# Kernel tuning notes

Measured on AMD Instinct MI355X. Metric: run time of the kernel, lower is better.

The kernel has to match this reference:

```python
import jax, jax.numpy as jnp
import numpy as np

B, S, D, O, C = 4, 2048, 1024, 1024, 8


def setup_inputs() -> dict:
    key = jax.random.key(0)
    k1, k2, k3, k4 = jax.random.split(key, 4)
    x = jax.random.normal(k1, (B, S, D), dtype=jnp.float32)
    category_id = jax.random.randint(k2, (B, S), 0, C, dtype=jnp.int64)
    weight = jax.random.normal(k3, (C, D, O), dtype=jnp.float32)
    bias = jax.random.normal(k4, (C, O), dtype=jnp.float32)
    return {"x": x, "category_id": category_id, "weight": weight, "bias": bias}


def reference(x, category_id, weight, bias):
    # Faithful to: out[t] = x[t] @ weight[cid[t]] + bias[cid[t]]
    # Instead of gathering a full [T, D, O] weight tensor per token (32GB),
    # compute every category's projection once and select per token.
    orig_shape = x.shape
    x_flat = x.reshape(-1, orig_shape[-1])          # [T, D]
    cid = category_id.reshape(-1)                    # [T]
    out_all = jnp.einsum('td,cdo->tco', x_flat, weight)  # [T, C, O]
    out = jnp.take_along_axis(out_all, cid[:, None, None], axis=1)[:, 0, :]  # [T, O]
    out = out + bias[cid]
    return out.reshape(orig_shape[:-1] + (weight.shape[-1],))
```

## Files before the change

### kernel.cpp

```cpp
#include <hip/hip_runtime.h>

#define TOK   8192
#define DIM   1024
#define OUTD  1024
#define NCAT  8
#define BM    128
#define BN    128
#define BK    32
#define NKT   (DIM / BK)
#define MAX_MT 71
#define MPMAX (MAX_MT * BM)

typedef __attribute__((ext_vector_type(8))) __bf16 bf16x8;
typedef __attribute__((ext_vector_type(4))) float  f32x4;

__device__ __forceinline__ unsigned short f2bf(float f) {
  unsigned u = __float_as_uint(f);
  u += 0x7fffu + ((u >> 16) & 1u);
  return (unsigned short)(u >> 16);
}

__global__ __launch_bounds__(1024) void k_build(const int* __restrict__ cid,
    int* __restrict__ row_token, int* __restrict__ tile_c, int* __restrict__ tile_m) {
  __shared__ int wcnt[16][NCAT];
  __shared__ int wbase[16][NCAT];
  __shared__ int gbase[NCAT];
  int tid = threadIdx.x, lane = tid & 63, wave = tid >> 6;
  int base = wave * 512;

  int cs[8];
  #pragma unroll
  for (int it = 0; it < 8; ++it) cs[it] = cid[base + it * 64 + lane];
  int cnt_loc[NCAT];
  #pragma unroll
  for (int c = 0; c < NCAT; ++c) cnt_loc[c] = 0;
  #pragma unroll
  for (int it = 0; it < 8; ++it) {
    #pragma unroll
    for (int c = 0; c < NCAT; ++c) {
      unsigned long long m = __ballot(cs[it] == c);
      cnt_loc[c] += __popcll(m);
    }
  }
  if (lane == 0) {
    #pragma unroll
    for (int c = 0; c < NCAT; ++c) wcnt[wave][c] = cnt_loc[c];
  }
  __syncthreads();

  if (tid == 0) {
    int pr = 0, mt = 0;
    for (int c = 0; c < NCAT; ++c) {
      int tot = 0;
      for (int w = 0; w < 16; ++w) { wbase[w][c] = tot; tot += wcnt[w][c]; }
      gbase[c] = pr;
      int nt = (tot + BM - 1) / BM;
      for (int i = 0; i < nt; ++i) { tile_c[mt] = c; tile_m[mt] = pr + i * BM; ++mt; }
      pr += nt * BM;
    }
    for (; mt < MAX_MT; ++mt) { tile_c[mt] = -1; tile_m[mt] = 0; }
  }
  __syncthreads();
  for (int r = tid; r < MPMAX; r += 1024) row_token[r] = -1;
  __syncthreads();

  int run[NCAT];
  #pragma unroll
  for (int c = 0; c < NCAT; ++c) run[c] = gbase[c] + wbase[wave][c];
  unsigned long long lt = (lane == 63) ? ~0ull >> 1 : ((1ull << lane) - 1);
  #pragma unroll
  for (int it = 0; it < 8; ++it) {
    int t = base + it * 64 + lane;
    int c = cs[it];
    int pos = 0;
    #pragma unroll
    for (int cat = 0; cat < NCAT; ++cat) {
      unsigned long long m = __ballot(cs[it] == cat);
      if (cat == c) pos = run[cat] + __popcll(m & lt);
      run[cat] += __popcll(m);
    }
    row_token[pos] = t;
  }
}

__global__ __launch_bounds__(256) void k_convert(const float* __restrict__ w,
    const float* __restrict__ x, const int* __restrict__ row_token,
    unsigned short* __restrict__ wt, unsigned short* __restrict__ xg) {
  int tid = threadIdx.x;
  if (blockIdx.x < 2048) {
    int b = blockIdx.x;
    int ot = b & 15, dt = (b >> 4) & 15, c = b >> 8;
    __shared__ unsigned short t[64][72];
    int i  = tid >> 2;
    int jg = tid & 3;
    const float* src = w + ((size_t)c << 20) + (size_t)(dt * 64 + i) * 1024 + ot * 64 + jg * 16;
    #pragma unroll
    for (int q = 0; q < 4; ++q) {
      float4 v = *(const float4*)(src + q * 4);
      t[jg * 16 + q * 4 + 0][i] = f2bf(v.x);
      t[jg * 16 + q * 4 + 1][i] = f2bf(v.y);
      t[jg * 16 + q * 4 + 2][i] = f2bf(v.z);
      t[jg * 16 + q * 4 + 3][i] = f2bf(v.w);
    }
    __syncthreads();
    unsigned short* dst = wt + ((size_t)c << 20) + (size_t)(ot * 64 + i) * 1024 + dt * 64 + jg * 16;
    uint4 a = *(const uint4*)&t[i][jg * 16];
    uint4 bq = *(const uint4*)&t[i][jg * 16 + 8];
    *(uint4*)dst = a;
    *(uint4*)(dst + 8) = bq;
  } else {
    int idx = (blockIdx.x - 2048) * 256 + tid;
    int r  = idx >> 7;
    int e0 = (idx & 127) << 3;
    if (r >= MPMAX) return;
    int tok = row_token[r];
    union { unsigned short u[8]; uint4 v; } o;
    if (tok >= 0) {
      const float4* s = (const float4*)(x + (size_t)tok * DIM + e0);
      float4 a = s[0], b = s[1];
      o.u[0] = f2bf(a.x); o.u[1] = f2bf(a.y); o.u[2] = f2bf(a.z); o.u[3] = f2bf(a.w);
      o.u[4] = f2bf(b.x); o.u[5] = f2bf(b.y); o.u[6] = f2bf(b.z); o.u[7] = f2bf(b.w);
    } else {
      o.v = make_uint4(0u, 0u, 0u, 0u);
    }
    *(uint4*)(xg + (size_t)r * DIM + e0) = o.v;
  }
}

__global__ __launch_bounds__(256) void k_gemm(const unsigned short* __restrict__ xg,
    const unsigned short* __restrict__ wt, const float* __restrict__ bias,
    const int* __restrict__ row_token, const int* __restrict__ tile_c,
    const int* __restrict__ tile_m, float* __restrict__ out) {
  int wg  = blockIdx.x;
  int lin = (wg & 7) * MAX_MT + (wg >> 3);
  int mt  = lin >> 3;
  int nt  = lin & 7;
  int c = tile_c[mt];
  if (c < 0) return;
  int m0 = tile_m[mt];
  int n0 = nt * BN;

  __shared__ unsigned short As[3][BM][BK];
  __shared__ unsigned short Bs[3][BM][BK];

  int tid  = threadIdx.x;
  int lane = tid & 63;
  int wr = (tid >> 6) >> 1, wc = (tid >> 6) & 1;

  f32x4 acc[4][4];
  #pragma unroll
  for (int m = 0; m < 4; ++m)
    #pragma unroll
    for (int n = 0; n < 4; ++n) acc[m][n] = (f32x4){0.f, 0.f, 0.f, 0.f};

  const unsigned short* Ag = xg + (size_t)m0 * DIM;
  const unsigned short* Bg = wt + ((size_t)c << 20) + (size_t)n0 * DIM;

  int srow = tid >> 2;
  int sdst = (tid & 3) << 3;
  int gsrc = (((tid & 3) ^ ((tid >> 3) & 3)) << 3);

  auto STAGE = [&](int b, int kt) {
    __builtin_amdgcn_global_load_lds(
      (const __attribute__((address_space(1))) unsigned int*)(Ag + (size_t)srow * DIM + kt + gsrc),
      (__attribute__((address_space(3))) unsigned int*)(&As[b][srow][sdst]), 16, 0, 0);
    __builtin_amdgcn_global_load_lds(
      (const __attribute__((address_space(1))) unsigned int*)(Ag + (size_t)(srow + 64) * DIM + kt + gsrc),
      (__attribute__((address_space(3))) unsigned int*)(&As[b][srow + 64][sdst]), 16, 0, 0);
    __builtin_amdgcn_global_load_lds(
      (const __attribute__((address_space(1))) unsigned int*)(Bg + (size_t)srow * DIM + kt + gsrc),
      (__attribute__((address_space(3))) unsigned int*)(&Bs[b][srow][sdst]), 16, 0, 0);
    __builtin_amdgcn_global_load_lds(
      (const __attribute__((address_space(1))) unsigned int*)(Bg + (size_t)(srow + 64) * DIM + kt + gsrc),
      (__attribute__((address_space(3))) unsigned int*)(&Bs[b][srow + 64][sdst]), 16, 0, 0);
  };

  int rcol = (((lane >> 4) ^ ((lane & 15) >> 1 & 3)) << 3);
  int arow = wr * 64 + (lane & 15);
  int brow = wc * 64 + (lane & 15);

  STAGE(0, 0); STAGE(1, BK); STAGE(2, 2 * BK);

  int b = 0;
  for (int t = 0; t < NKT; ++t) {
    if (t < NKT - 2)       asm volatile("s_waitcnt vmcnt(8)" ::: "memory");
    else if (t == NKT - 2) asm volatile("s_waitcnt vmcnt(4)" ::: "memory");
    else                   asm volatile("s_waitcnt vmcnt(0)" ::: "memory");
    __builtin_amdgcn_s_barrier();

    bf16x8 af[4], bf[4];
    #pragma unroll
    for (int m = 0; m < 4; ++m)
      af[m] = *(const bf16x8*)&As[b][arow + m * 16][rcol];
    #pragma unroll
    for (int n = 0; n < 4; ++n)
      bf[n] = *(const bf16x8*)&Bs[b][brow + n * 16][rcol];
    #pragma unroll
    for (int m = 0; m < 4; ++m)
      #pragma unroll
      for (int n = 0; n < 4; ++n)
        acc[m][n] = __builtin_amdgcn_mfma_f32_16x16x32_bf16(af[m], bf[n], acc[m][n], 0, 0, 0);

    __builtin_amdgcn_s_barrier();
    if (t < NKT - 3) STAGE(b, (t + 3) * BK);
    b = (b == 2) ? 0 : b + 1;
  }

  int col = lane & 15;
  int rq  = (lane >> 4) << 2;
  float bv[4];
  #pragma unroll
  for (int n = 0; n < 4; ++n) bv[n] = bias[c * OUTD + n0 + wc * 64 + n * 16 + col];
  #pragma unroll
  for (int m = 0; m < 4; ++m) {
    #pragma unroll
    for (int r = 0; r < 4; ++r) {
      int prow = m0 + wr * 64 + m * 16 + rq + r;
      int tok = row_token[prow];
      if (tok < 0) continue;
      float* orow = out + (size_t)tok * OUTD + n0 + wc * 64 + col;
      #pragma unroll
      for (int n = 0; n < 4; ++n) orow[n * 16] = acc[m][n][r] + bv[n];
    }
  }
}

extern "C" void kernel_launch(void* const* d_in, const int* in_sizes, int n_in,
                              void* d_out, int out_size, void* d_ws, size_t ws_size,
                              hipStream_t stream) {
  const float* x    = (const float*)d_in[0];
  const int*   cid  = (const int*)d_in[1];
  const float* w    = (const float*)d_in[2];
  const float* bias = (const float*)d_in[3];
  float* out = (float*)d_out;

  char* ws = (char*)d_ws;
  constexpr size_t XG_BYTES = (size_t)MPMAX * DIM * 2;
  constexpr size_t WT_BYTES = (size_t)NCAT * DIM * OUTD * 2;
  constexpr size_t RT_BYTES = (size_t)MPMAX * 4;
  unsigned short* xg  = (unsigned short*)ws;
  unsigned short* wtb = (unsigned short*)(ws + XG_BYTES);
  int* row_token = (int*)(ws + XG_BYTES + WT_BYTES);
  int* tile_c    = (int*)(ws + XG_BYTES + WT_BYTES + RT_BYTES);
  int* tile_m    = tile_c + MAX_MT;

  k_build<<<1, 1024, 0, stream>>>(cid, row_token, tile_c, tile_m);
  k_convert<<<2048 + (MPMAX * (DIM / 8) + 255) / 256, 256, 0, stream>>>(w, x, row_token, wtb, xg);
  k_gemm<<<8 * MAX_MT, 256, 0, stream>>>(xg, wtb, bias, row_token, tile_c, tile_m, out);
}
```

Baseline: 151.0 us.

## Fuse x gather and bf16 conversion into GEMM A-tile loads, merge prep kernels

New measurement: 177.9 us. 17.8% more time.

```diff
diff --git a/kernel.cpp b/kernel.cpp
--- a/kernel.cpp
+++ b/kernel.cpp
@@ -20,72 +20,9 @@
   return (unsigned short)(u >> 16);
 }
 
-__global__ __launch_bounds__(1024) void k_build(const int* __restrict__ cid,
+__global__ __launch_bounds__(256) void k_prep(const float* __restrict__ w,
+    const int* __restrict__ cid, unsigned short* __restrict__ wt,
     int* __restrict__ row_token, int* __restrict__ tile_c, int* __restrict__ tile_m) {
-  __shared__ int wcnt[16][NCAT];
-  __shared__ int wbase[16][NCAT];
-  __shared__ int gbase[NCAT];
-  int tid = threadIdx.x, lane = tid & 63, wave = tid >> 6;
-  int base = wave * 512;
-
-  int cs[8];
-  #pragma unroll
-  for (int it = 0; it < 8; ++it) cs[it] = cid[base + it * 64 + lane];
-  int cnt_loc[NCAT];
-  #pragma unroll
-  for (int c = 0; c < NCAT; ++c) cnt_loc[c] = 0;
-  #pragma unroll
-  for (int it = 0; it < 8; ++it) {
-    #pragma unroll
-    for (int c = 0; c < NCAT; ++c) {
-      unsigned long long m = __ballot(cs[it] == c);
-      cnt_loc[c] += __popcll(m);
-    }
-  }
-  if (lane == 0) {
-    #pragma unroll
-    for (int c = 0; c < NCAT; ++c) wcnt[wave][c] = cnt_loc[c];
-  }
-  __syncthreads();
-
-  if (tid == 0) {
-    int pr = 0, mt = 0;
-    for (int c = 0; c < NCAT; ++c) {
-      int tot = 0;
-      for (int w = 0; w < 16; ++w) { wbase[w][c] = tot; tot += wcnt[w][c]; }
-      gbase[c] = pr;
-      int nt = (tot + BM - 1) / BM;
-      for (int i = 0; i < nt; ++i) { tile_c[mt] = c; tile_m[mt] = pr + i * BM; ++mt; }
-      pr += nt * BM;
-    }
-    for (; mt < MAX_MT; ++mt) { tile_c[mt] = -1; tile_m[mt] = 0; }
-  }
-  __syncthreads();
-  for (int r = tid; r < MPMAX; r += 1024) row_token[r] = -1;
-  __syncthreads();
-
-  int run[NCAT];
-  #pragma unroll
-  for (int c = 0; c < NCAT; ++c) run[c] = gbase[c] + wbase[wave][c];
-  unsigned long long lt = (lane == 63) ? ~0ull >> 1 : ((1ull << lane) - 1);
-  #pragma unroll
-  for (int it = 0; it < 8; ++it) {
-    int t = base + it * 64 + lane;
-    int c = cs[it];
-    int pos = 0;
-    #pragma unroll
-    for (int cat = 0; cat < NCAT; ++cat) {
-      unsigned long long m = __ballot(cs[it] == cat);
-      if (cat == c) pos = run[cat] + __popcll(m & lt);
-      run[cat] += __popcll(m);
-    }
-    row_token[pos] = t;
-  }
-}
-
-__global__ __launch_bounds__(256) void k_convert(const float* __restrict__ w,
-    const float* __restrict__ x, const int* __restrict__ row_token,
-    unsigned short* __restrict__ wt, unsigned short* __restrict__ xg) {
   int tid = threadIdx.x;
   if (blockIdx.x < 2048) {
     int b = blockIdx.x;
@@ -108,26 +45,67 @@
     uint4 bq = *(const uint4*)&t[i][jg * 16 + 8];
     *(uint4*)dst = a;
     *(uint4*)(dst + 8) = bq;
-  } else {
-    int idx = (blockIdx.x - 2048) * 256 + tid;
-    int r  = idx >> 7;
-    int e0 = (idx & 127) << 3;
-    if (r >= MPMAX) return;
-    int tok = row_token[r];
-    union { unsigned short u[8]; uint4 v; } o;
-    if (tok >= 0) {
-      const float4* s = (const float4*)(x + (size_t)tok * DIM + e0);
-      float4 a = s[0], b = s[1];
-      o.u[0] = f2bf(a.x); o.u[1] = f2bf(a.y); o.u[2] = f2bf(a.z); o.u[3] = f2bf(a.w);
-      o.u[4] = f2bf(b.x); o.u[5] = f2bf(b.y); o.u[6] = f2bf(b.z); o.u[7] = f2bf(b.w);
-    } else {
-      o.v = make_uint4(0u, 0u, 0u, 0u);
-    }
-    *(uint4*)(xg + (size_t)r * DIM + e0) = o.v;
-  }
-}
-
-__global__ __launch_bounds__(256) void k_gemm(const unsigned short* __restrict__ xg,
+    return;
+  }
+
+  __shared__ int wcnt[4][NCAT];
+  __shared__ int wbase[4][NCAT];
+  __shared__ int gbase[NCAT];
+  int lane = tid & 63, wave = tid >> 6;
+  int base = wave * 2048;
+
+  int cs[32];
+  #pragma unroll
+  for (int it = 0; it < 32; ++it) cs[it] = cid[base + it * 64 + lane];
+  int cnt_loc[NCAT];
+  #pragma unroll
+  for (int c = 0; c < NCAT; ++c) cnt_loc[c] = 0;
+  #pragma unroll
+  for (int it = 0; it < 32; ++it)
+    #pragma unroll
+    for (int c = 0; c < NCAT; ++c)
+      cnt_loc[c] += __popcll(__ballot(cs[it] == c));
+  if (lane == 0) {
+    #pragma unroll
+    for (int c = 0; c < NCAT; ++c) wcnt[wave][c] = cnt_loc[c];
+  }
+  __syncthreads();
+
+  if (tid == 0) {
+    int pr = 0, mt = 0;
+    for (int c = 0; c < NCAT; ++c) {
+      int tot = 0;
+      for (int wv = 0; wv < 4; ++wv) { wbase[wv][c] = tot; tot += wcnt[wv][c]; }
+      gbase[c] = pr;
+      int nt = (tot + BM - 1) / BM;
+      for (int i = 0; i < nt; ++i) { tile_c[mt] = c; tile_m[mt] = pr + i * BM; ++mt; }
+      pr += nt * BM;
+    }
+    for (; mt < MAX_MT; ++mt) { tile_c[mt] = -1; tile_m[mt] = 0; }
+  }
+  __syncthreads();
+  for (int r = tid; r < MPMAX; r += 256) row_token[r] = -1;
+  __syncthreads();
+
+  int run[NCAT];
+  #pragma unroll
+  for (int c = 0; c < NCAT; ++c) run[c] = gbase[c] + wbase[wave][c];
+  unsigned long long lt = (lane == 63) ? ~0ull >> 1 : ((1ull << lane) - 1);
+  #pragma unroll
+  for (int it = 0; it < 32; ++it) {
+    int c = cs[it];
+    int pos = 0;
+    #pragma unroll
+    for (int cat = 0; cat < NCAT; ++cat) {
+      unsigned long long m = __ballot(cs[it] == cat);
+      if (cat == c) pos = run[cat] + __popcll(m & lt);
+      run[cat] += __popcll(m);
+    }
+    row_token[pos] = base + it * 64 + lane;
+  }
+}
+
+__global__ __launch_bounds__(256) void k_gemm(const float* __restrict__ x,
     const unsigned short* __restrict__ wt, const float* __restrict__ bias,
     const int* __restrict__ row_token, const int* __restrict__ tile_c,
     const int* __restrict__ tile_m, float* __restrict__ out) {
@@ -140,8 +118,8 @@
   int m0 = tile_m[mt];
   int n0 = nt * BN;
 
-  __shared__ unsigned short As[3][BM][BK];
-  __shared__ unsigned short Bs[3][BM][BK];
+  __shared__ unsigned short As[2][BM][BK];
+  __shared__ unsigned short Bs[2][BM][BK];
 
   int tid  = threadIdx.x;
   int lane = tid & 63;
@@ -153,20 +131,39 @@
     #pragma unroll
     for (int n = 0; n < 4; ++n) acc[m][n] = (f32x4){0.f, 0.f, 0.f, 0.f};
 
-  const unsigned short* Ag = xg + (size_t)m0 * DIM;
-  const unsigned short* Bg = wt + ((size_t)c << 20) + (size_t)n0 * DIM;
+  int arowS = tid >> 1;
+  int khalf = (tid & 1) << 4;
+  int tk = row_token[m0 + arowS];
+  bool avalid = tk >= 0;
+  const float* xs = x + (size_t)(avalid ? tk : 0) * DIM + khalf;
+  int g0   = (tid & 1) << 1;
+  int aswz = (arowS >> 1) & 3;
+  int a0 = ((g0 ^ aswz) << 3);
+  int a1 = (((g0 + 1) ^ aswz) << 3);
 
   int srow = tid >> 2;
   int sdst = (tid & 3) << 3;
   int gsrc = (((tid & 3) ^ ((tid >> 3) & 3)) << 3);
-
-  auto STAGE = [&](int b, int kt) {
-    __builtin_amdgcn_global_load_lds(
-      (const __attribute__((address_space(1))) unsigned int*)(Ag + (size_t)srow * DIM + kt + gsrc),
-      (__attribute__((address_space(3))) unsigned int*)(&As[b][srow][sdst]), 16, 0, 0);
-    __builtin_amdgcn_global_load_lds(
-      (const __attribute__((address_space(1))) unsigned int*)(Ag + (size_t)(srow + 64) * DIM + kt + gsrc),
-      (__attribute__((address_space(3))) unsigned int*)(&As[b][srow + 64][sdst]), 16, 0, 0);
+  const unsigned short* Bg = wt + ((size_t)c << 20) + (size_t)n0 * DIM;
+
+  float4 v0, v1, v2, v3;
+  auto LOADA = [&](int kt) {
+    v0 = *(const float4*)(xs + kt);
+    v1 = *(const float4*)(xs + kt + 4);
+    v2 = *(const float4*)(xs + kt + 8);
+    v3 = *(const float4*)(xs + kt + 12);
+  };
+  auto WRITEA = [&](int b) {
+    bf16x8 p0, p1;
+    p0[0] = (__bf16)v0.x; p0[1] = (__bf16)v0.y; p0[2] = (__bf16)v0.z; p0[3] = (__bf16)v0.w;
+    p0[4] = (__bf16)v1.x; p0[5] = (__bf16)v1.y; p0[6] = (__bf16)v1.z; p0[7] = (__bf16)v1.w;
+    p1[0] = (__bf16)v2.x; p1[1] = (__bf16)v2.y; p1[2] = (__bf16)v2.z; p1[3] = (__bf16)v2.w;
+    p1[4] = (__bf16)v3.x; p1[5] = (__bf16)v3.y; p1[6] = (__bf16)v3.z; p1[7] = (__bf16)v3.w;
+    if (!avalid) { p0 = (bf16x8){}; p1 = (bf16x8){}; }
+    *(bf16x8*)&As[b][arowS][a0] = p0;
+    *(bf16x8*)&As[b][arowS][a1] = p1;
+  };
+  auto STAGEB = [&](int b, int kt) {
     __builtin_amdgcn_global_load_lds(
       (const __attribute__((address_space(1))) unsigned int*)(Bg + (size_t)srow * DIM + kt + gsrc),
       (__attribute__((address_space(3))) unsigned int*)(&Bs[b][srow][sdst]), 16, 0, 0);
@@ -175,35 +172,36 @@
       (__attribute__((address_space(3))) unsigned int*)(&Bs[b][srow + 64][sdst]), 16, 0, 0);
   };
 
-  int rcol = (((lane >> 4) ^ ((lane & 15) >> 1 & 3)) << 3);
+  int rcol = (((lane >> 4) ^ (((lane & 15) >> 1) & 3)) << 3);
   int arow = wr * 64 + (lane & 15);
   int brow = wc * 64 + (lane & 15);
 
-  STAGE(0, 0); STAGE(1, BK); STAGE(2, 2 * BK);
-
-  int b = 0;
+  LOADA(0);
+  STAGEB(0, 0);
+  WRITEA(0);
+  __syncthreads();
+
+  int cur = 0;
   for (int t = 0; t < NKT; ++t) {
-    if (t < NKT - 2)       asm volatile("s_waitcnt vmcnt(8)" ::: "memory");
-    else if (t == NKT - 2) asm volatile("s_waitcnt vmcnt(4)" ::: "memory");
-    else                   asm volatile("s_waitcnt vmcnt(0)" ::: "memory");
-    __builtin_amdgcn_s_barrier();
+    bool pre = (t + 1 < NKT);
+    if (pre) { LOADA((t + 1) * BK); STAGEB(cur ^ 1, (t + 1) * BK); }
 
     bf16x8 af[4], bf[4];
     #pragma unroll
     for (int m = 0; m < 4; ++m)
-      af[m] = *(const bf16x8*)&As[b][arow + m * 16][rcol];
+      af[m] = *(const bf16x8*)&As[cur][arow + m * 16][rcol];
     #pragma unroll
     for (int n = 0; n < 4; ++n)
-      bf[n] = *(const bf16x8*)&Bs[b][brow + n * 16][rcol];
+      bf[n] = *(const bf16x8*)&Bs[cur][brow + n * 16][rcol];
     #pragma unroll
     for (int m = 0; m < 4; ++m)
       #pragma unroll
       for (int n = 0; n < 4; ++n)
         acc[m][n] = __builtin_amdgcn_mfma_f32_16x16x32_bf16(af[m], bf[n], acc[m][n], 0, 0, 0);
 
-    __builtin_amdgcn_s_barrier();
-    if (t < NKT - 3) STAGE(b, (t + 3) * BK);
-    b = (b == 2) ? 0 : b + 1;
+    if (pre) WRITEA(cur ^ 1);
+    __syncthreads();
+    cur ^= 1;
   }
 
   int col = lane & 15;
@@ -235,16 +233,13 @@
   float* out = (float*)d_out;
 
   char* ws = (char*)d_ws;
-  constexpr size_t XG_BYTES = (size_t)MPMAX * DIM * 2;
   constexpr size_t WT_BYTES = (size_t)NCAT * DIM * OUTD * 2;
   constexpr size_t RT_BYTES = (size_t)MPMAX * 4;
-  unsigned short* xg  = (unsigned short*)ws;
-  unsigned short* wtb = (unsigned short*)(ws + XG_BYTES);
-  int* row_token = (int*)(ws + XG_BYTES + WT_BYTES);
-  int* tile_c    = (int*)(ws + XG_BYTES + WT_BYTES + RT_BYTES);
+  unsigned short* wtb = (unsigned short*)ws;
+  int* row_token = (int*)(ws + WT_BYTES);
+  int* tile_c    = (int*)(ws + WT_BYTES + RT_BYTES);
   int* tile_m    = tile_c + MAX_MT;
 
-  k_build<<<1, 1024, 0, stream>>>(cid, row_token, tile_c, tile_m);
-  k_convert<<<2048 + (MPMAX * (DIM / 8) + 255) / 256, 256, 0, stream>>>(w, x, row_token, wtb, xg);
-  k_gemm<<<8 * MAX_MT, 256, 0, stream>>>(xg, wtb, bias, row_token, tile_c, tile_m, out);
-}
+  k_prep<<<2049, 256, 0, stream>>>(w, cid, wtb, row_token, tile_c, tile_m);
+  k_gemm<<<8 * MAX_MT, 256, 0, stream>>>(x, wtb, bias, row_token, tile_c, tile_m, out);
+}
```
